# Optimization experiments

Hardware: AMD Instinct MI355X
Metric: run time of the kernel (lower is better)

Reference implementation:

```python
import jax, jax.numpy as jnp
import numpy as np

# Kornia's fixed 5x5 pyramid (binomial) kernel used by build_pyramid/pyrdown
_PYR_K = np.array([[1, 4, 6, 4, 1],
                   [4, 16, 24, 16, 4],
                   [6, 24, 36, 24, 6],
                   [4, 16, 24, 16, 4],
                   [1, 4, 6, 4, 1]], dtype=np.float32) / 256.0


def _pyrdown(x):
    """kornia pyrdown: 5x5 binomial blur (reflect pad) + bilinear resize to (H//2, W//2)."""
    B, C, H, W = x.shape
    xp = jnp.pad(x, ((0, 0), (0, 0), (2, 2), (2, 2)), mode='reflect')
    k = jnp.broadcast_to(jnp.asarray(_PYR_K, x.dtype), (C, 1, 5, 5))  # depthwise
    y = jax.lax.conv_general_dilated(
        xp, k, window_strides=(1, 1), padding='VALID',
        feature_group_count=C, dimension_numbers=('NCHW', 'OIHW', 'NCHW'))
    # torch F.interpolate bilinear align_corners=False == jax resize bilinear, antialias off
    return jax.image.resize(y, (B, C, H // 2, W // 2), method='bilinear', antialias=False)


def _norm_pc(x):
    """Per-channel min-max normalization to [0,1] over spatial dims."""
    mx = jnp.max(x, axis=(2, 3), keepdims=True)
    mn = jnp.min(x, axis=(2, 3), keepdims=True)
    return (x - mn) / (mx - mn)


def _avg_local_max(x):
    """Mean of 16x16 tile maxima; torch loop range(0, H-16, 16) skips the last tile
    row/col, and with zero tiles the torch code yields nan_to_num(0/0) == 0."""
    B, C, H, W = x.shape
    s = 16
    ny = len(range(0, H - s, s))
    nx = len(range(0, W - s, s))
    if ny == 0 or nx == 0:
        return jnp.zeros((B, C, 1, 1), x.dtype)
    t = x[:, :, :ny * s, :nx * s].reshape(B, C, ny, s, nx, s)
    lmax = jnp.max(t, axis=(3, 5))           # [B,C,ny,nx]
    return jnp.mean(lmax, axis=(2, 3)).reshape(B, C, 1, 1)


def _sm_normalization(x):
    d = _norm_pc(x)
    lm = _avg_local_max(d)
    return d * (1.0 - lm) ** 2


def setup_inputs() -> dict:
    key = jax.random.key(0)
    x = jax.random.normal(key, (8, 3, 512, 512), dtype=jnp.float32)
    return {"x": x}


def reference(x):
    B, C, H, W = x.shape
    inp = _norm_pc(x)
    max_level = int(H).bit_length() - 1   # 9 for H=512
    u = max_level - 1

    # Gaussian pyramid of length max_level: [inp, pyrdown(inp), ...]
    pyr = [inp]
    for _ in range(max_level - 1):
        pyr.append(_pyrdown(pyr[-1]))

    acc = None
    for i in range(u - 1):
        h, w = pyr[i + 1].shape[2], pyr[i + 1].shape[3]
        up = jnp.repeat(jnp.repeat(pyr[i + 2], 2, axis=2), 2, axis=3)[:, :, :h, :w]
        d = jnp.abs(pyr[i + 1] - up)
        nd = jax.image.resize(_sm_normalization(d), (B, C, H, W),
                              method='bilinear', antialias=False)
        acc = nd if acc is None else acc + nd

    return jnp.mean(acc, axis=1)  # [B,H,W]
```

## Files before the change

kernel.cpp:

```cpp
#include <hip/hip_runtime.h>
#include <math.h>

#define NPLANES 24
#define FINF 3.402823466e38f

__host__ __device__ __forceinline__ int d_off(int li) {
    return 2097152 - (2097152 >> (2 * li));
}

__device__ __forceinline__ int refl(int v, int S) {
    if (v < 0) v = -v;
    if (v >= S) v = 2 * S - 2 - v;
    return v;
}

__device__ __forceinline__ float wmin64(float v) {
#pragma unroll
    for (int o = 32; o > 0; o >>= 1) v = fminf(v, __shfl_down(v, o, 64));
    return v;
}
__device__ __forceinline__ float wmax64(float v) {
#pragma unroll
    for (int o = 32; o > 0; o >>= 1) v = fmaxf(v, __shfl_down(v, o, 64));
    return v;
}
__device__ __forceinline__ float wsum64(float v) {
#pragma unroll
    for (int o = 32; o > 0; o >>= 1) v += __shfl_down(v, o, 64);
    return v;
}
__device__ __forceinline__ float bmin1024(float v, float* cross, int tid) {
    v = wmin64(v);
    if ((tid & 63) == 0) cross[tid >> 6] = v;
    __syncthreads();
    if (tid < 16) {
        float t = cross[tid];
#pragma unroll
        for (int o = 8; o > 0; o >>= 1) t = fminf(t, __shfl_down(t, o, 16));
        if (tid == 0) cross[0] = t;
    }
    __syncthreads();
    float r = cross[0];
    __syncthreads();
    return r;
}
__device__ __forceinline__ float bmax1024(float v, float* cross, int tid) {
    v = wmax64(v);
    if ((tid & 63) == 0) cross[tid >> 6] = v;
    __syncthreads();
    if (tid < 16) {
        float t = cross[tid];
#pragma unroll
        for (int o = 8; o > 0; o >>= 1) t = fmaxf(t, __shfl_down(t, o, 16));
        if (tid == 0) cross[0] = t;
    }
    __syncthreads();
    float r = cross[0];
    __syncthreads();
    return r;
}
__device__ __forceinline__ float bsum1024(float v, float* cross, int tid) {
    v = wsum64(v);
    if ((tid & 63) == 0) cross[tid >> 6] = v;
    __syncthreads();
    if (tid < 16) {
        float t = cross[tid];
#pragma unroll
        for (int o = 8; o > 0; o >>= 1) t += __shfl_down(t, o, 16);
        if (tid == 0) cross[0] = t;
    }
    __syncthreads();
    float r = cross[0];
    __syncthreads();
    return r;
}

__device__ __forceinline__ float stencil6(const float* s, int S, int i, int j) {
    const float w[6] = {1.f, 5.f, 10.f, 10.f, 5.f, 1.f};
    int rx[6];
#pragma unroll
    for (int b = 0; b < 6; ++b) rx[b] = refl(2 * j - 2 + b, S);
    float acc = 0.f;
#pragma unroll
    for (int a = 0; a < 6; ++a) {
        int ry = refl(2 * i - 2 + a, S);
        const float* rp = s + ry * S;
        float r = 0.f;
#pragma unroll
        for (int b = 0; b < 6; ++b) r += w[b] * rp[rx[b]];
        acc += w[a] * r;
    }
    return acc * (1.f / 1024.f);
}

template <int IS, bool HAS_D>
__global__ __launch_bounds__(256) void pyrdown_tiled(const float* __restrict__ in,
                                                     float* __restrict__ out,
                                                     float* __restrict__ dout,
                                                     float* __restrict__ tileMin,
                                                     float* __restrict__ tileMax) {
    constexpr int SO = IS / 2;
    constexpr int TO = 32;
    constexpr int TI = 2 * TO + 4;
    constexpr int TPA = SO / TO;
    __shared__ float sIn[TI * TI];
    __shared__ float sH[TI * TO];
    __shared__ float sOut[TO * TO];
    __shared__ float sD[HAS_D ? 64 * 65 : 1];
    __shared__ float rmn[HAS_D ? 256 : 1], rmx[HAS_D ? 256 : 1];

    const int tid = threadIdx.x;
    const int p = blockIdx.x / (TPA * TPA);
    const int t = blockIdx.x % (TPA * TPA);
    const int ty = t / TPA, tx = t % TPA;
    const int oy = ty * TO, ox = tx * TO;
    const int iy = 2 * oy - 2, ix = 2 * ox - 2;
    const float* ip = in + (size_t)p * IS * IS;

    for (int k = tid; k < TI * TI; k += 256) {
        int r = k / TI, c = k - r * TI;
        sIn[k] = ip[refl(iy + r, IS) * IS + refl(ix + c, IS)];
    }
    __syncthreads();

    for (int k = tid; k < TI * 8; k += 256) {
        int r = k >> 3, jq = k & 7;
        const float4* rp = (const float4*)(sIn + r * TI + 8 * jq);
        float4 v0 = rp[0], v1 = rp[1], v2 = rp[2];
        float4 o;
        o.x = v0.x + 5.f * v0.y + 10.f * v0.z + 10.f * v0.w + 5.f * v1.x + v1.y;
        o.y = v0.z + 5.f * v0.w + 10.f * v1.x + 10.f * v1.y + 5.f * v1.z + v1.w;
        o.z = v1.x + 5.f * v1.y + 10.f * v1.z + 10.f * v1.w + 5.f * v2.x + v2.y;
        o.w = v1.z + 5.f * v1.w + 10.f * v2.x + 10.f * v2.y + 5.f * v2.z + v2.w;
        *(float4*)(sH + r * TO + 4 * jq) = o;
    }
    __syncthreads();

    {
        int i = tid >> 3, jq = tid & 7;
        const float* base = sH + (2 * i) * TO + 4 * jq;
        float4 r0 = *(const float4*)(base);
        float4 r1 = *(const float4*)(base + TO);
        float4 r2 = *(const float4*)(base + 2 * TO);
        float4 r3 = *(const float4*)(base + 3 * TO);
        float4 r4 = *(const float4*)(base + 4 * TO);
        float4 r5 = *(const float4*)(base + 5 * TO);
        float4 o;
        o.x = (r0.x + 5.f * r1.x + 10.f * r2.x + 10.f * r3.x + 5.f * r4.x + r5.x) * (1.f / 1024.f);
        o.y = (r0.y + 5.f * r1.y + 10.f * r2.y + 10.f * r3.y + 5.f * r4.y + r5.y) * (1.f / 1024.f);
        o.z = (r0.z + 5.f * r1.z + 10.f * r2.z + 10.f * r3.z + 5.f * r4.z + r5.z) * (1.f / 1024.f);
        o.w = (r0.w + 5.f * r1.w + 10.f * r2.w + 10.f * r3.w + 5.f * r4.w + r5.w) * (1.f / 1024.f);
        *(float4*)(sOut + i * TO + 4 * jq) = o;
        *(float4*)(out + (size_t)p * SO * SO + (size_t)(oy + i) * SO + ox + 4 * jq) = o;
    }

    if (HAS_D) {
        __syncthreads();
        float* dp = dout + (size_t)p * IS * IS;
        for (int k = tid; k < 4096; k += 256) {
            int yy = k >> 6, xx = k & 63;
            float dv = fabsf(sIn[(yy + 2) * TI + xx + 2] - sOut[(yy >> 1) * TO + (xx >> 1)]);
            sD[yy * 65 + xx] = dv;
            dp[(size_t)(2 * oy + yy) * IS + 2 * ox + xx] = dv;
        }
        __syncthreads();
        int s = tid >> 4, r = tid & 15;
        int tr = s >> 2, tc = s & 3;
        const float* rowp = sD + (tr * 16 + r) * 65 + tc * 16;
        float mn = FINF, mx = -FINF;
#pragma unroll
        for (int c = 0; c < 16; ++c) {
            float v = rowp[c];
            mn = fminf(mn, v); mx = fmaxf(mx, v);
        }
        rmn[tid] = mn; rmx[tid] = mx;
        __syncthreads();
        for (int st = 8; st > 0; st >>= 1) {
            if (r < st) {
                rmn[tid] = fminf(rmn[tid], rmn[tid + st]);
                rmx[tid] = fmaxf(rmx[tid], rmx[tid + st]);
            }
            __syncthreads();
        }
        if (r == 0) {
            constexpr int TA = IS / 16;
            int gidx = p * TA * TA + (ty * 4 + tr) * TA + (tx * 4 + tc);
            tileMin[gidx] = rmn[tid];
            tileMax[gidx] = rmx[tid];
        }
    }
}

__global__ __launch_bounds__(1024) void fused_small_kernel(const float* __restrict__ pyr2,
                                                           float* __restrict__ dBase,
                                                           const float* __restrict__ tileMin,
                                                           const float* __restrict__ tileMax,
                                                           float* __restrict__ A,
                                                           float* __restrict__ B) {
    __shared__ float sP2[16384];
    __shared__ float sHbuf[8192];
    __shared__ float sP3[4096];
    __shared__ float cross[16];
    __shared__ float strip[1024];
    __shared__ float tmaxLds[64];
    float* sd2 = sHbuf;
    float* sp4 = sHbuf + 4096;
    float* sd3 = sHbuf + 5120;
    float* sp5 = sHbuf + 6144;
    float* sd4 = sHbuf + 6400;
    float* sp6 = sHbuf + 6656;
    float* sd5 = sHbuf + 6720;
    float* sp7 = sHbuf + 6784;
    float* sd6 = sHbuf + 6800;
    const int tid = threadIdx.x;
    const int p = blockIdx.x;

    {
        const float4* gp = (const float4*)(pyr2 + (size_t)p * 16384);
        float4* sv = (float4*)sP2;
        for (int k = tid; k < 4096; k += 1024) sv[k] = gp[k];
    }
    __syncthreads();
    for (int k = tid; k < 8192; k += 1024) {
        int r = k >> 6, c = k & 63;
        int b0 = 2 * c - 2;
        const float* rp = sP2 + r * 128;
        sHbuf[k] = rp[refl(b0, 128)] + 5.f * rp[refl(b0 + 1, 128)] + 10.f * rp[refl(b0 + 2, 128)] +
                   10.f * rp[refl(b0 + 3, 128)] + 5.f * rp[refl(b0 + 4, 128)] + rp[refl(b0 + 5, 128)];
    }
    __syncthreads();
    for (int k = tid; k < 4096; k += 1024) {
        int r3 = k >> 6, c = k & 63;
        int b0 = 2 * r3 - 2;
        float s = sHbuf[refl(b0, 128) * 64 + c] + 5.f * sHbuf[refl(b0 + 1, 128) * 64 + c] +
                  10.f * sHbuf[refl(b0 + 2, 128) * 64 + c] + 10.f * sHbuf[refl(b0 + 3, 128) * 64 + c] +
                  5.f * sHbuf[refl(b0 + 4, 128) * 64 + c] + sHbuf[refl(b0 + 5, 128) * 64 + c];
        sP3[k] = s * (1.f / 1024.f);
    }
    __syncthreads();
    float mnReg = FINF, mxReg = -FINF;
    {
        float4* d1g = (float4*)(dBase + d_off(1) + (size_t)p * 16384);
        float4* sv = (float4*)sP2;
        for (int k = tid; k < 4096; k += 1024) {
            int row = k >> 5, c4 = k & 31;
            float4 v = sv[k];
            float2 o = *(const float2*)(sP3 + (row >> 1) * 64 + 2 * c4);
            float4 dv;
            dv.x = fabsf(v.x - o.x);
            dv.y = fabsf(v.y - o.x);
            dv.z = fabsf(v.z - o.y);
            dv.w = fabsf(v.w - o.y);
            sv[k] = dv;
            d1g[k] = dv;
            mnReg = fminf(mnReg, fminf(fminf(dv.x, dv.y), fminf(dv.z, dv.w)));
            mxReg = fmaxf(mxReg, fmaxf(fmaxf(dv.x, dv.y), fmaxf(dv.z, dv.w)));
        }
    }
    __syncthreads();
    {
        float mn = bmin1024(mnReg, cross, tid);
        float mx = bmax1024(mxReg, cross, tid);
        {
            int s = tid >> 4, r = tid & 15;
            int tr = s >> 3, tc = s & 7;
            const float4* rowp = (const float4*)(sP2 + (tr * 16 + r) * 128 + tc * 16);
            float sm = -FINF;
#pragma unroll
            for (int q = 0; q < 4; ++q) {
                float4 v = rowp[q];
                sm = fmaxf(sm, fmaxf(fmaxf(v.x, v.y), fmaxf(v.z, v.w)));
            }
            strip[tid] = sm;
        }
        __syncthreads();
        if (tid < 64) {
            float tm = -FINF;
            for (int r = 0; r < 16; ++r) tm = fmaxf(tm, strip[tid * 16 + r]);
            tmaxLds[tid] = tm;
        }
        __syncthreads();
        float su = (tid < 64 && (tid >> 3) < 7 && (tid & 7) < 7) ? tmaxLds[tid] : 0.f;
        float sum = bsum1024(su, cross, tid);
        if (tid == 0) {
            float inv = 1.f / (mx - mn);
            float lm = (sum * (1.f / 49.f) - mn) * inv;
            float g = (1.f - lm) * (1.f - lm);
            A[1 * NPLANES + p] = g * inv;
            B[1 * NPLANES + p] = -mn * g * inv;
        }
    }
    {
        float tmn = (tid < 256) ? tileMin[p * 256 + tid] : FINF;
        float tmx = (tid < 256) ? tileMax[p * 256 + tid] : -FINF;
        float mn = bmin1024(tmn, cross, tid);
        float mx = bmax1024(tmx, cross, tid);
        float su = (tid < 256 && (tid >> 4) < 15 && (tid & 15) < 15) ? tmx : 0.f;
        float sum = bsum1024(su, cross, tid);
        if (tid == 0) {
            float inv = 1.f / (mx - mn);
            float lm = (sum * (1.f / 225.f) - mn) * inv;
            float g = (1.f - lm) * (1.f - lm);
            A[0 * NPLANES + p] = g * inv;
            B[0 * NPLANES + p] = -mn * g * inv;
        }
    }
    __syncthreads();

    {
        float* d2g = dBase + d_off(2) + (size_t)p * 4096;
        int i = tid >> 5, j = tid & 31;
        float v = stencil6(sP3, 64, i, j);
        sp4[tid] = v;
#pragma unroll
        for (int di = 0; di < 2; ++di)
#pragma unroll
            for (int dj = 0; dj < 2; ++dj) {
                int y = 2 * i + di, x = 2 * j + dj;
                float dv = fabsf(sP3[y * 64 + x] - v);
                sd2[y * 64 + x] = dv;
                d2g[y * 64 + x] = dv;
            }
    }
    __syncthreads();
    if (tid < 256) {
        int i = tid >> 4, j = tid & 15;
        float v = stencil6(sp4, 32, i, j);
        sp5[tid] = v;
        float* d3g = dBase + d_off(3) + (size_t)p * 1024;
#pragma unroll
        for (int di = 0; di < 2; ++di)
#pragma unroll
            for (int dj = 0; dj < 2; ++dj) {
                int y = 2 * i + di, x = 2 * j + dj;
                float dv = fabsf(sp4[y * 32 + x] - v);
                sd3[y * 32 + x] = dv;
                d3g[y * 32 + x] = dv;
            }
    }
    __syncthreads();
    if (tid < 64) {
        int i = tid >> 3, j = tid & 7;
        float v = stencil6(sp5, 16, i, j);
        sp6[tid] = v;
        float* d4g = dBase + d_off(4) + (size_t)p * 256;
#pragma unroll
        for (int di = 0; di < 2; ++di)
#pragma unroll
            for (int dj = 0; dj < 2; ++dj) {
                int y = 2 * i + di, x = 2 * j + dj;
                float dv = fabsf(sp5[y * 16 + x] - v);
                sd4[y * 16 + x] = dv;
                d4g[y * 16 + x] = dv;
            }
    }
    __syncthreads();
    if (tid < 16) {
        int i = tid >> 2, j = tid & 3;
        float v = stencil6(sp6, 8, i, j);
        sp7[tid] = v;
        float* d5g = dBase + d_off(5) + (size_t)p * 64;
#pragma unroll
        for (int di = 0; di < 2; ++di)
#pragma unroll
            for (int dj = 0; dj < 2; ++dj) {
                int y = 2 * i + di, x = 2 * j + dj;
                float dv = fabsf(sp6[y * 8 + x] - v);
                sd5[y * 8 + x] = dv;
                d5g[y * 8 + x] = dv;
            }
    }
    __syncthreads();
    if (tid < 4) {
        int i = tid >> 1, j = tid & 1;
        float v = stencil6(sp7, 4, i, j);
        float* d6g = dBase + d_off(6) + (size_t)p * 16;
#pragma unroll
        for (int di = 0; di < 2; ++di)
#pragma unroll
            for (int dj = 0; dj < 2; ++dj) {
                int y = 2 * i + di, x = 2 * j + dj;
                float dv = fabsf(sp7[y * 4 + x] - v);
                sd6[y * 4 + x] = dv;
                d6g[y * 4 + x] = dv;
            }
    }
    __syncthreads();

    {
        float4 q = ((const float4*)sd2)[tid];
        float mn = fminf(fminf(q.x, q.y), fminf(q.z, q.w));
        float mx = fmaxf(fmaxf(q.x, q.y), fmaxf(q.z, q.w));
        mn = bmin1024(mn, cross, tid);
        mx = bmax1024(mx, cross, tid);
        if (tid < 256) {
            int t = tid >> 4, r = tid & 15;
            int ty = t >> 2, tx = t & 3;
            const float* rowp = sd2 + (ty * 16 + r) * 64 + tx * 16;
            float sm = -FINF;
#pragma unroll
            for (int c = 0; c < 16; ++c) sm = fmaxf(sm, rowp[c]);
            strip[tid] = sm;
        }
        __syncthreads();
        if (tid < 16) {
            float tm = -FINF;
            for (int r = 0; r < 16; ++r) tm = fmaxf(tm, strip[tid * 16 + r]);
            tmaxLds[tid] = tm;
        }
        __syncthreads();
        if (tid == 0) {
            float s = 0.f;
            for (int ty = 0; ty < 3; ++ty)
                for (int tx = 0; tx < 3; ++tx) s += tmaxLds[ty * 4 + tx];
            float inv = 1.f / (mx - mn);
            float lm = (s * (1.f / 9.f) - mn) * inv;
            float g = (1.f - lm) * (1.f - lm);
            A[2 * NPLANES + p] = g * inv;
            B[2 * NPLANES + p] = -mn * g * inv;
        }
        __syncthreads();
    }
    {
        float v = sd3[tid];
        float mn = bmin1024(v, cross, tid);
        float mx = bmax1024(v, cross, tid);
        float e = (tid < 256) ? sd3[(tid >> 4) * 32 + (tid & 15)] : -FINF;
        float tm = bmax1024(e, cross, tid);
        if (tid == 0) {
            float inv = 1.f / (mx - mn);
            float lm = (tm - mn) * inv;
            float g = (1.f - lm) * (1.f - lm);
            A[3 * NPLANES + p] = g * inv;
            B[3 * NPLANES + p] = -mn * g * inv;
        }
    }
    {
        float v = (tid < 256) ? sd4[tid] : FINF;
        float mn = bmin1024(v, cross, tid);
        v = (tid < 256) ? sd4[tid] : -FINF;
        float mx = bmax1024(v, cross, tid);
        if (tid == 0) {
            float inv = 1.f / (mx - mn);
            A[4 * NPLANES + p] = inv; B[4 * NPLANES + p] = -mn * inv;
        }
    }
    {
        float v = (tid < 64) ? sd5[tid] : FINF;
        float mn = bmin1024(v, cross, tid);
        v = (tid < 64) ? sd5[tid] : -FINF;
        float mx = bmax1024(v, cross, tid);
        if (tid == 0) {
            float inv = 1.f / (mx - mn);
            A[5 * NPLANES + p] = inv; B[5 * NPLANES + p] = -mn * inv;
        }
    }
    {
        float v = (tid < 16) ? sd6[tid] : FINF;
        float mn = bmin1024(v, cross, tid);
        v = (tid < 16) ? sd6[tid] : -FINF;
        float mx = bmax1024(v, cross, tid);
        if (tid == 0) {
            float inv = 1.f / (mx - mn);
            A[6 * NPLANES + p] = inv; B[6 * NPLANES + p] = -mn * inv;
        }
    }
}

__global__ __launch_bounds__(256) void final_kernel(const float* __restrict__ dBase,
                                                    const float* __restrict__ A,
                                                    const float* __restrict__ Bc,
                                                    float* __restrict__ out) {
    __shared__ float patch[1700];
    __shared__ float sBtot;
    const int tid = threadIdx.x;
    const int b = blockIdx.x >> 6;
    const int tile = blockIdx.x & 63;
    const int yb = (tile >> 3) << 6;
    const int xb = (tile & 7) << 6;

    if (tid == 0) {
        float s = 0.f;
        for (int k = 0; k < 7; ++k)
            for (int c = 0; c < 3; ++c) s += Bc[k * NPLANES + b * 3 + c];
        sBtot = s;
    }

    const int dims[7] = {34, 18, 10, 6, 4, 3, 3};
    const int lofs[7] = {0, 1156, 1480, 1580, 1616, 1632, 1641};
    int baseY[7], baseX[7];
#pragma unroll
    for (int li = 0; li < 7; ++li) {
        const int S = 256 >> li;
        const float s = 1.f / (float)(2 << li);
        baseY[li] = (int)floorf((yb + 0.5f) * s - 0.5f);
        baseX[li] = (int)floorf((xb + 0.5f) * s - 0.5f);
        const int dim = dims[li];
        const int n = dim * dim;
        const float* d0p = dBase + d_off(li) + (size_t)(b * 3) * S * S;
        const float* d1p = d0p + S * S;
        const float* d2p = d1p + S * S;
        const float A0 = A[li * NPLANES + b * 3 + 0];
        const float A1 = A[li * NPLANES + b * 3 + 1];
        const float A2 = A[li * NPLANES + b * 3 + 2];
        for (int k = tid; k < n; k += 256) {
            int r = k / dim, c = k - r * dim;
            int sr = min(max(baseY[li] + r, 0), S - 1);
            int sc = min(max(baseX[li] + c, 0), S - 1);
            int si = sr * S + sc;
            patch[lofs[li] + k] = A0 * d0p[si] + A1 * d1p[si] + A2 * d2p[si];
        }
    }
    __syncthreads();

    const int ty = tid >> 4, tx = tid & 15;
    const int gy0 = yb + (ty << 2), gx0 = xb + (tx << 2);
    float acc[4][4];
#pragma unroll
    for (int i = 0; i < 4; ++i)
#pragma unroll
        for (int j = 0; j < 4; ++j) acc[i][j] = 0.f;

    {
        const int dim = 34;
        float wy[4], wx[4];
        int ry[4], cx[4];
#pragma unroll
        for (int k = 0; k < 4; ++k) {
            float fy = (gy0 + k + 0.5f) * 0.5f - 0.5f;
            float fl = floorf(fy);
            wy[k] = fy - fl; ry[k] = (int)fl - baseY[0];
            float fx = (gx0 + k + 0.5f) * 0.5f - 0.5f;
            fl = floorf(fx);
            wx[k] = fx - fl; cx[k] = (int)fl - baseX[0];
        }
        const int r0 = ry[0], c0 = cx[0];
        const float* pp = patch + r0 * dim + c0;
        float P[4][4];
#pragma unroll
        for (int r = 0; r < 4; ++r)
#pragma unroll
            for (int c = 0; c < 4; ++c) P[r][c] = pp[r * dim + c];
        float h[4][4];
#pragma unroll
        for (int j = 0; j < 4; ++j) {
            int dx = cx[j] - c0;
#pragma unroll
            for (int r = 0; r < 4; ++r) {
                float a = dx == 0 ? P[r][0] : (dx == 1 ? P[r][1] : P[r][2]);
                float bb = dx == 0 ? P[r][1] : (dx == 1 ? P[r][2] : P[r][3]);
                h[r][j] = a + wx[j] * (bb - a);
            }
        }
#pragma unroll
        for (int i = 0; i < 4; ++i) {
            int dy = ry[i] - r0;
#pragma unroll
            for (int j = 0; j < 4; ++j) {
                float h0 = dy == 0 ? h[0][j] : (dy == 1 ? h[1][j] : h[2][j]);
                float h1 = dy == 0 ? h[1][j] : (dy == 1 ? h[2][j] : h[3][j]);
                acc[i][j] += h0 + wy[i] * (h1 - h0);
            }
        }
    }
#pragma unroll
    for (int li = 1; li < 7; ++li) {
        const int dim = dims[li];
        const float* P0 = patch + lofs[li];
        const float s = 1.f / (float)(2 << li);
        float wy[4], wx[4];
        int ry[4], cx[4];
#pragma unroll
        for (int k = 0; k < 4; ++k) {
            float fy = (gy0 + k + 0.5f) * s - 0.5f;
            float fl = floorf(fy);
            wy[k] = fy - fl; ry[k] = (int)fl - baseY[li];
            float fx = (gx0 + k + 0.5f) * s - 0.5f;
            fl = floorf(fx);
            wx[k] = fx - fl; cx[k] = (int)fl - baseX[li];
        }
        const int r0 = ry[0], c0 = cx[0];
        const float* pp = P0 + r0 * dim + c0;
        float P[3][3];
#pragma unroll
        for (int r = 0; r < 3; ++r)
#pragma unroll
            for (int c = 0; c < 3; ++c) P[r][c] = pp[r * dim + c];
        float h[3][4];
#pragma unroll
        for (int j = 0; j < 4; ++j) {
            int dx = cx[j] - c0;
#pragma unroll
            for (int r = 0; r < 3; ++r) {
                float a = dx == 0 ? P[r][0] : P[r][1];
                float bb = dx == 0 ? P[r][1] : P[r][2];
                h[r][j] = a + wx[j] * (bb - a);
            }
        }
#pragma unroll
        for (int i = 0; i < 4; ++i) {
            int dy = ry[i] - r0;
#pragma unroll
            for (int j = 0; j < 4; ++j) {
                float h0 = dy == 0 ? h[0][j] : h[1][j];
                float h1 = dy == 0 ? h[1][j] : h[2][j];
                acc[i][j] += h0 + wy[i] * (h1 - h0);
            }
        }
    }

    const float bt = sBtot;
    float* op = out + ((size_t)b * 512 + gy0) * 512 + gx0;
#pragma unroll
    for (int i = 0; i < 4; ++i) {
        float4 v;
        v.x = (acc[i][0] + bt) * (1.f / 3.f);
        v.y = (acc[i][1] + bt) * (1.f / 3.f);
        v.z = (acc[i][2] + bt) * (1.f / 3.f);
        v.w = (acc[i][3] + bt) * (1.f / 3.f);
        *(float4*)(op + (size_t)i * 512) = v;
    }
}

extern "C" void kernel_launch(void* const* d_in, const int* in_sizes, int n_in,
                              void* d_out, int out_size, void* d_ws, size_t ws_size,
                              hipStream_t stream) {
    (void)in_sizes; (void)n_in; (void)out_size; (void)ws_size;
    const float* x = (const float*)d_in[0];
    float* ws = (float*)d_ws;
    float* out = (float*)d_out;

    float* pyr1 = ws;
    float* pyr2 = ws + 1572864;
    float* dBase = ws + 1966080;
    float* tileMin = ws + 4063104;
    float* tileMax = ws + 4069248;
    float* A = ws + 4075392;
    float* Bc = ws + 4075560;

    pyrdown_tiled<512, false><<<NPLANES * 64, 256, 0, stream>>>(x, pyr1, nullptr, nullptr, nullptr);
    pyrdown_tiled<256, true><<<NPLANES * 16, 256, 0, stream>>>(pyr1, pyr2, dBase + d_off(0), tileMin, tileMax);
    fused_small_kernel<<<NPLANES, 1024, 0, stream>>>(pyr2, dBase, tileMin, tileMax, A, Bc);
    final_kernel<<<8 * 64, 256, 0, stream>>>(dBase, A, Bc, out);
}
```

Measured before the change: 116.5 us.

## Replace block-wide reductions with per-wave reductions and overlap pyramid tail with stats

Removes the 1024-thread block reductions (each with three barriers) and assigns each plane's min/max/tile-max statistics to a single wavefront using xor shuffles. The small pyramid levels 3-6 are computed by one wave while other waves concurrently compute level-1 and level-2 statistics, collapsing many __syncthreads into two. This cuts barrier count and idle threads in the fused small-level kernel, at the cost of serialising small-level stencils onto one wave.

```diff
diff --git a/kernel.cpp b/kernel.cpp
--- a/kernel.cpp
+++ b/kernel.cpp
@@ -14,65 +14,17 @@
     return v;
 }
 
-__device__ __forceinline__ float wmin64(float v) {
-#pragma unroll
-    for (int o = 32; o > 0; o >>= 1) v = fminf(v, __shfl_down(v, o, 64));
+__device__ __forceinline__ void wminmax64(float& mn, float& mx) {
+#pragma unroll
+    for (int o = 32; o > 0; o >>= 1) {
+        mn = fminf(mn, __shfl_xor(mn, o, 64));
+        mx = fmaxf(mx, __shfl_xor(mx, o, 64));
+    }
+}
+__device__ __forceinline__ float wsumx64(float v) {
+#pragma unroll
+    for (int o = 32; o > 0; o >>= 1) v += __shfl_xor(v, o, 64);
     return v;
-}
-__device__ __forceinline__ float wmax64(float v) {
-#pragma unroll
-    for (int o = 32; o > 0; o >>= 1) v = fmaxf(v, __shfl_down(v, o, 64));
-    return v;
-}
-__device__ __forceinline__ float wsum64(float v) {
-#pragma unroll
-    for (int o = 32; o > 0; o >>= 1) v += __shfl_down(v, o, 64);
-    return v;
-}
-__device__ __forceinline__ float bmin1024(float v, float* cross, int tid) {
-    v = wmin64(v);
-    if ((tid & 63) == 0) cross[tid >> 6] = v;
-    __syncthreads();
-    if (tid < 16) {
-        float t = cross[tid];
-#pragma unroll
-        for (int o = 8; o > 0; o >>= 1) t = fminf(t, __shfl_down(t, o, 16));
-        if (tid == 0) cross[0] = t;
-    }
-    __syncthreads();
-    float r = cross[0];
-    __syncthreads();
-    return r;
-}
-__device__ __forceinline__ float bmax1024(float v, float* cross, int tid) {
-    v = wmax64(v);
-    if ((tid & 63) == 0) cross[tid >> 6] = v;
-    __syncthreads();
-    if (tid < 16) {
-        float t = cross[tid];
-#pragma unroll
-        for (int o = 8; o > 0; o >>= 1) t = fmaxf(t, __shfl_down(t, o, 16));
-        if (tid == 0) cross[0] = t;
-    }
-    __syncthreads();
-    float r = cross[0];
-    __syncthreads();
-    return r;
-}
-__device__ __forceinline__ float bsum1024(float v, float* cross, int tid) {
-    v = wsum64(v);
-    if ((tid & 63) == 0) cross[tid >> 6] = v;
-    __syncthreads();
-    if (tid < 16) {
-        float t = cross[tid];
-#pragma unroll
-        for (int o = 8; o > 0; o >>= 1) t += __shfl_down(t, o, 16);
-        if (tid == 0) cross[0] = t;
-    }
-    __syncthreads();
-    float r = cross[0];
-    __syncthreads();
-    return r;
 }
 
 __device__ __forceinline__ float stencil6(const float* s, int S, int i, int j) {
@@ -200,9 +152,6 @@
     __shared__ float sP2[16384];
     __shared__ float sHbuf[8192];
     __shared__ float sP3[4096];
-    __shared__ float cross[16];
-    __shared__ float strip[1024];
-    __shared__ float tmaxLds[64];
     float* sd2 = sHbuf;
     float* sp4 = sHbuf + 4096;
     float* sd3 = sHbuf + 5120;
@@ -238,7 +187,6 @@
         sP3[k] = s * (1.f / 1024.f);
     }
     __syncthreads();
-    float mnReg = FINF, mxReg = -FINF;
     {
         float4* d1g = (float4*)(dBase + d_off(1) + (size_t)p * 16384);
         float4* sv = (float4*)sP2;
@@ -253,51 +201,135 @@
             dv.w = fabsf(v.w - o.y);
             sv[k] = dv;
             d1g[k] = dv;
-            mnReg = fminf(mnReg, fminf(fminf(dv.x, dv.y), fminf(dv.z, dv.w)));
-            mxReg = fmaxf(mxReg, fmaxf(fmaxf(dv.x, dv.y), fmaxf(dv.z, dv.w)));
         }
     }
     __syncthreads();
     {
-        float mn = bmin1024(mnReg, cross, tid);
-        float mx = bmax1024(mxReg, cross, tid);
+        float* d2g = dBase + d_off(2) + (size_t)p * 4096;
+        int i = tid >> 5, j = tid & 31;
+        float v = stencil6(sP3, 64, i, j);
+        sp4[tid] = v;
+#pragma unroll
+        for (int di = 0; di < 2; ++di)
+#pragma unroll
+            for (int dj = 0; dj < 2; ++dj) {
+                int y = 2 * i + di, x = 2 * j + dj;
+                float dv = fabsf(sP3[y * 64 + x] - v);
+                sd2[y * 64 + x] = dv;
+                d2g[y * 64 + x] = dv;
+            }
+    }
+    __syncthreads();
+
+    const int wave = tid >> 6, lane = tid & 63;
+
+    if (wave == 0) {
+        float* d3g = dBase + d_off(3) + (size_t)p * 1024;
+#pragma unroll
+        for (int q = 0; q < 4; ++q) {
+            int k = lane + 64 * q;
+            int i = k >> 4, j = k & 15;
+            float v = stencil6(sp4, 32, i, j);
+            sp5[k] = v;
+#pragma unroll
+            for (int di = 0; di < 2; ++di)
+#pragma unroll
+                for (int dj = 0; dj < 2; ++dj) {
+                    int y = 2 * i + di, x = 2 * j + dj;
+                    float dv = fabsf(sp4[y * 32 + x] - v);
+                    sd3[y * 32 + x] = dv;
+                    d3g[y * 32 + x] = dv;
+                }
+        }
         {
-            int s = tid >> 4, r = tid & 15;
-            int tr = s >> 3, tc = s & 7;
-            const float4* rowp = (const float4*)(sP2 + (tr * 16 + r) * 128 + tc * 16);
-            float sm = -FINF;
-#pragma unroll
-            for (int q = 0; q < 4; ++q) {
-                float4 v = rowp[q];
-                sm = fmaxf(sm, fmaxf(fmaxf(v.x, v.y), fmaxf(v.z, v.w)));
-            }
-            strip[tid] = sm;
-        }
-        __syncthreads();
-        if (tid < 64) {
+            int i = lane >> 3, j = lane & 7;
+            float v = stencil6(sp5, 16, i, j);
+            sp6[lane] = v;
+            float* d4g = dBase + d_off(4) + (size_t)p * 256;
+#pragma unroll
+            for (int di = 0; di < 2; ++di)
+#pragma unroll
+                for (int dj = 0; dj < 2; ++dj) {
+                    int y = 2 * i + di, x = 2 * j + dj;
+                    float dv = fabsf(sp5[y * 16 + x] - v);
+                    sd4[y * 16 + x] = dv;
+                    d4g[y * 16 + x] = dv;
+                }
+        }
+        if (lane < 16) {
+            int i = lane >> 2, j = lane & 3;
+            float v = stencil6(sp6, 8, i, j);
+            sp7[lane] = v;
+            float* d5g = dBase + d_off(5) + (size_t)p * 64;
+#pragma unroll
+            for (int di = 0; di < 2; ++di)
+#pragma unroll
+                for (int dj = 0; dj < 2; ++dj) {
+                    int y = 2 * i + di, x = 2 * j + dj;
+                    float dv = fabsf(sp6[y * 8 + x] - v);
+                    sd5[y * 8 + x] = dv;
+                    d5g[y * 8 + x] = dv;
+                }
+        }
+        if (lane < 4) {
+            int i = lane >> 1, j = lane & 1;
+            float v = stencil6(sp7, 4, i, j);
+            float* d6g = dBase + d_off(6) + (size_t)p * 16;
+#pragma unroll
+            for (int di = 0; di < 2; ++di)
+#pragma unroll
+                for (int dj = 0; dj < 2; ++dj) {
+                    int y = 2 * i + di, x = 2 * j + dj;
+                    float dv = fabsf(sp7[y * 4 + x] - v);
+                    sd6[y * 4 + x] = dv;
+                    d6g[y * 4 + x] = dv;
+                }
+        }
+    } else if (wave == 1) {
+        const float4* sv = (const float4*)sP2;
+        float mn = FINF, mx = -FINF;
+        for (int k = lane; k < 4096; k += 64) {
+            float4 v = sv[k];
+            mn = fminf(mn, fminf(fminf(v.x, v.y), fminf(v.z, v.w)));
+            mx = fmaxf(mx, fmaxf(fmaxf(v.x, v.y), fmaxf(v.z, v.w)));
+        }
+        wminmax64(mn, mx);
+        float tmax = 0.f;
+        if (lane < 49) {
+            int tr = lane / 7, tc = lane % 7;
+            const float4* base = (const float4*)(sP2 + (tr * 16) * 128 + tc * 16);
             float tm = -FINF;
-            for (int r = 0; r < 16; ++r) tm = fmaxf(tm, strip[tid * 16 + r]);
-            tmaxLds[tid] = tm;
-        }
-        __syncthreads();
-        float su = (tid < 64 && (tid >> 3) < 7 && (tid & 7) < 7) ? tmaxLds[tid] : 0.f;
-        float sum = bsum1024(su, cross, tid);
-        if (tid == 0) {
+            for (int r = 0; r < 16; ++r) {
+#pragma unroll
+                for (int c = 0; c < 4; ++c) {
+                    float4 v = base[r * 32 + c];
+                    tm = fmaxf(tm, fmaxf(fmaxf(v.x, v.y), fmaxf(v.z, v.w)));
+                }
+            }
+            tmax = tm;
+        }
+        float sum = wsumx64(tmax);
+        if (lane == 0) {
             float inv = 1.f / (mx - mn);
             float lm = (sum * (1.f / 49.f) - mn) * inv;
             float g = (1.f - lm) * (1.f - lm);
             A[1 * NPLANES + p] = g * inv;
             B[1 * NPLANES + p] = -mn * g * inv;
         }
-    }
-    {
-        float tmn = (tid < 256) ? tileMin[p * 256 + tid] : FINF;
-        float tmx = (tid < 256) ? tileMax[p * 256 + tid] : -FINF;
-        float mn = bmin1024(tmn, cross, tid);
-        float mx = bmax1024(tmx, cross, tid);
-        float su = (tid < 256 && (tid >> 4) < 15 && (tid & 15) < 15) ? tmx : 0.f;
-        float sum = bsum1024(su, cross, tid);
-        if (tid == 0) {
+    } else if (wave == 2) {
+        float mn = FINF, mx = -FINF, su = 0.f;
+#pragma unroll
+        for (int q = 0; q < 4; ++q) {
+            int t = lane + 64 * q;
+            float tmn = tileMin[p * 256 + t];
+            float tmx = tileMax[p * 256 + t];
+            mn = fminf(mn, tmn);
+            mx = fmaxf(mx, tmx);
+            if ((t >> 4) < 15 && (t & 15) < 15) su += tmx;
+        }
+        wminmax64(mn, mx);
+        float sum = wsumx64(su);
+        if (lane == 0) {
             float inv = 1.f / (mx - mn);
             float lm = (sum * (1.f / 225.f) - mn) * inv;
             float g = (1.f - lm) * (1.f - lm);
@@ -307,160 +339,84 @@
     }
     __syncthreads();
 
-    {
-        float* d2g = dBase + d_off(2) + (size_t)p * 4096;
-        int i = tid >> 5, j = tid & 31;
-        float v = stencil6(sP3, 64, i, j);
-        sp4[tid] = v;
-#pragma unroll
-        for (int di = 0; di < 2; ++di)
-#pragma unroll
-            for (int dj = 0; dj < 2; ++dj) {
-                int y = 2 * i + di, x = 2 * j + dj;
-                float dv = fabsf(sP3[y * 64 + x] - v);
-                sd2[y * 64 + x] = dv;
-                d2g[y * 64 + x] = dv;
-            }
-    }
-    __syncthreads();
-    if (tid < 256) {
-        int i = tid >> 4, j = tid & 15;
-        float v = stencil6(sp4, 32, i, j);
-        sp5[tid] = v;
-        float* d3g = dBase + d_off(3) + (size_t)p * 1024;
-#pragma unroll
-        for (int di = 0; di < 2; ++di)
-#pragma unroll
-            for (int dj = 0; dj < 2; ++dj) {
-                int y = 2 * i + di, x = 2 * j + dj;
-                float dv = fabsf(sp4[y * 32 + x] - v);
-                sd3[y * 32 + x] = dv;
-                d3g[y * 32 + x] = dv;
-            }
-    }
-    __syncthreads();
-    if (tid < 64) {
-        int i = tid >> 3, j = tid & 7;
-        float v = stencil6(sp5, 16, i, j);
-        sp6[tid] = v;
-        float* d4g = dBase + d_off(4) + (size_t)p * 256;
-#pragma unroll
-        for (int di = 0; di < 2; ++di)
-#pragma unroll
-            for (int dj = 0; dj < 2; ++dj) {
-                int y = 2 * i + di, x = 2 * j + dj;
-                float dv = fabsf(sp5[y * 16 + x] - v);
-                sd4[y * 16 + x] = dv;
-                d4g[y * 16 + x] = dv;
-            }
-    }
-    __syncthreads();
-    if (tid < 16) {
-        int i = tid >> 2, j = tid & 3;
-        float v = stencil6(sp6, 8, i, j);
-        sp7[tid] = v;
-        float* d5g = dBase + d_off(5) + (size_t)p * 64;
-#pragma unroll
-        for (int di = 0; di < 2; ++di)
-#pragma unroll
-            for (int dj = 0; dj < 2; ++dj) {
-                int y = 2 * i + di, x = 2 * j + dj;
-                float dv = fabsf(sp6[y * 8 + x] - v);
-                sd5[y * 8 + x] = dv;
-                d5g[y * 8 + x] = dv;
-            }
-    }
-    __syncthreads();
-    if (tid < 4) {
-        int i = tid >> 1, j = tid & 1;
-        float v = stencil6(sp7, 4, i, j);
-        float* d6g = dBase + d_off(6) + (size_t)p * 16;
-#pragma unroll
-        for (int di = 0; di < 2; ++di)
-#pragma unroll
-            for (int dj = 0; dj < 2; ++dj) {
-                int y = 2 * i + di, x = 2 * j + dj;
-                float dv = fabsf(sp7[y * 4 + x] - v);
-                sd6[y * 4 + x] = dv;
-                d6g[y * 4 + x] = dv;
-            }
-    }
-    __syncthreads();
-
-    {
-        float4 q = ((const float4*)sd2)[tid];
-        float mn = fminf(fminf(q.x, q.y), fminf(q.z, q.w));
-        float mx = fmaxf(fmaxf(q.x, q.y), fmaxf(q.z, q.w));
-        mn = bmin1024(mn, cross, tid);
-        mx = bmax1024(mx, cross, tid);
-        if (tid < 256) {
-            int t = tid >> 4, r = tid & 15;
-            int ty = t >> 2, tx = t & 3;
-            const float* rowp = sd2 + (ty * 16 + r) * 64 + tx * 16;
-            float sm = -FINF;
-#pragma unroll
-            for (int c = 0; c < 16; ++c) sm = fmaxf(sm, rowp[c]);
-            strip[tid] = sm;
-        }
-        __syncthreads();
-        if (tid < 16) {
-            float tm = -FINF;
-            for (int r = 0; r < 16; ++r) tm = fmaxf(tm, strip[tid * 16 + r]);
-            tmaxLds[tid] = tm;
-        }
-        __syncthreads();
-        if (tid == 0) {
-            float s = 0.f;
-            for (int ty = 0; ty < 3; ++ty)
-                for (int tx = 0; tx < 3; ++tx) s += tmaxLds[ty * 4 + tx];
+    if (wave == 0) {
+        const float4* sv = (const float4*)sd2;
+        float mn = FINF, mx = -FINF;
+#pragma unroll
+        for (int q = 0; q < 16; ++q) {
+            float4 v = sv[lane + 64 * q];
+            mn = fminf(mn, fminf(fminf(v.x, v.y), fminf(v.z, v.w)));
+            mx = fmaxf(mx, fmaxf(fmaxf(v.x, v.y), fmaxf(v.z, v.w)));
+        }
+        wminmax64(mn, mx);
+        float tmax = -FINF;
+        if (lane < 36) {
+            int t = lane >> 2, r4 = lane & 3;
+            int tr = t / 3, tc = t % 3;
+#pragma unroll
+            for (int rr = 0; rr < 4; ++rr) {
+                const float4* base = (const float4*)(sd2 + (16 * tr + 4 * r4 + rr) * 64 + 16 * tc);
+#pragma unroll
+                for (int c = 0; c < 4; ++c) {
+                    float4 v = base[c];
+                    tmax = fmaxf(tmax, fmaxf(fmaxf(v.x, v.y), fmaxf(v.z, v.w)));
+                }
+            }
+        }
+        tmax = fmaxf(tmax, __shfl_xor(tmax, 1, 64));
+        tmax = fmaxf(tmax, __shfl_xor(tmax, 2, 64));
+        float val = ((lane & 3) == 0 && lane < 36) ? tmax : 0.f;
+        float s = wsumx64(val);
+        if (lane == 0) {
             float inv = 1.f / (mx - mn);
             float lm = (s * (1.f / 9.f) - mn) * inv;
             float g = (1.f - lm) * (1.f - lm);
             A[2 * NPLANES + p] = g * inv;
             B[2 * NPLANES + p] = -mn * g * inv;
         }
-        __syncthreads();
-    }
-    {
-        float v = sd3[tid];
-        float mn = bmin1024(v, cross, tid);
-        float mx = bmax1024(v, cross, tid);
-        float e = (tid < 256) ? sd3[(tid >> 4) * 32 + (tid & 15)] : -FINF;
-        float tm = bmax1024(e, cross, tid);
-        if (tid == 0) {
+    } else if (wave == 1) {
+        const float4* sv = (const float4*)sd3;
+        float mn = FINF, mx = -FINF;
+#pragma unroll
+        for (int q = 0; q < 4; ++q) {
+            float4 v = sv[lane + 64 * q];
+            mn = fminf(mn, fminf(fminf(v.x, v.y), fminf(v.z, v.w)));
+            mx = fmaxf(mx, fmaxf(fmaxf(v.x, v.y), fmaxf(v.z, v.w)));
+        }
+        wminmax64(mn, mx);
+        float4 e4 = sv[(lane >> 2) * 8 + (lane & 3)];
+        float e = fmaxf(fmaxf(e4.x, e4.y), fmaxf(e4.z, e4.w));
+        float tn = e, tm = e;
+        wminmax64(tn, tm);
+        if (lane == 0) {
             float inv = 1.f / (mx - mn);
             float lm = (tm - mn) * inv;
             float g = (1.f - lm) * (1.f - lm);
             A[3 * NPLANES + p] = g * inv;
             B[3 * NPLANES + p] = -mn * g * inv;
         }
-    }
-    {
-        float v = (tid < 256) ? sd4[tid] : FINF;
-        float mn = bmin1024(v, cross, tid);
-        v = (tid < 256) ? sd4[tid] : -FINF;
-        float mx = bmax1024(v, cross, tid);
-        if (tid == 0) {
+    } else if (wave == 2) {
+        float4 v = ((const float4*)sd4)[lane];
+        float mn = fminf(fminf(v.x, v.y), fminf(v.z, v.w));
+        float mx = fmaxf(fmaxf(v.x, v.y), fmaxf(v.z, v.w));
+        wminmax64(mn, mx);
+        if (lane == 0) {
             float inv = 1.f / (mx - mn);
             A[4 * NPLANES + p] = inv; B[4 * NPLANES + p] = -mn * inv;
         }
-    }
-    {
-        float v = (tid < 64) ? sd5[tid] : FINF;
-        float mn = bmin1024(v, cross, tid);
-        v = (tid < 64) ? sd5[tid] : -FINF;
-        float mx = bmax1024(v, cross, tid);
-        if (tid == 0) {
+    } else if (wave == 3) {
+        float v = sd5[lane];
+        float mn = v, mx = v;
+        wminmax64(mn, mx);
+        if (lane == 0) {
             float inv = 1.f / (mx - mn);
             A[5 * NPLANES + p] = inv; B[5 * NPLANES + p] = -mn * inv;
         }
-    }
-    {
-        float v = (tid < 16) ? sd6[tid] : FINF;
-        float mn = bmin1024(v, cross, tid);
-        v = (tid < 16) ? sd6[tid] : -FINF;
-        float mx = bmax1024(v, cross, tid);
-        if (tid == 0) {
+    } else if (wave == 4) {
+        float v = (lane < 16) ? sd6[lane] : sd6[0];
+        float mn = v, mx = v;
+        wminmax64(mn, mx);
+        if (lane == 0) {
             float inv = 1.f / (mx - mn);
             A[6 * NPLANES + p] = inv; B[6 * NPLANES + p] = -mn * inv;
         }
```

Result: faster. 109.4 us (-6.1%).
